# Kernel optimization log

Hardware: AMD Instinct MI355X
Metric: run time of the kernel (lower is better)

The kernel has to match this reference:

```python
import jax, jax.numpy as jnp
import numpy as np

UNITS = 256   # wiring.units (state size)
OUT = 64      # wiring.output_dim (motor neurons = last OUT units)


def setup_inputs() -> dict:
    key = jax.random.key(0)
    k_x, k_wi, k_wr, k_mi, k_mr = jax.random.split(key, 5)
    B, L, C = 32, 8192, 128
    x = jax.random.normal(k_x, (B, L, C), dtype=jnp.float32)
    # learned parameters
    W_in = jax.random.normal(k_wi, (C, UNITS), dtype=jnp.float32) * 0.05
    W_rec = jax.random.normal(k_wr, (UNITS, UNITS), dtype=jnp.float32) * 0.05
    b = jnp.zeros((UNITS,), dtype=jnp.float32)
    # fixed sparse wiring masks (sensory adjacency [C,U], recurrent adjacency [U,U])
    M_in = jax.random.bernoulli(k_mi, 0.5, (C, UNITS)).astype(jnp.float32)
    M_rec = jax.random.bernoulli(k_mr, 0.5, (UNITS, UNITS)).astype(jnp.float32)
    return {"x": x, "W_in": W_in, "W_rec": W_rec, "b": b, "M_in": M_in, "M_rec": M_rec}


def reference(x, W_in, W_rec, b, M_in, M_rec):
    # Pre-apply the wiring sparsity masks once (original masks weights each step).
    Wi = W_in * M_in          # [C, U]
    Wr = W_rec * M_rec        # [U, U]
    B = x.shape[0]
    h0 = jnp.zeros((B, UNITS), dtype=x.dtype)
    xT = jnp.swapaxes(x, 0, 1)  # [L, B, C] -> scan over time

    def step(h, xt):
        h_new = jnp.tanh(xt @ Wi + h @ Wr + b)   # wired RNN cell, tanh nonlinearity
        # output_size < state_size: emit only motor neurons (last OUT units)
        return h_new, h_new[:, UNITS - OUT:]

    h_last, ys = jax.lax.scan(step, h0, xT)      # ys: [L, B, OUT]
    readout = jnp.swapaxes(ys, 0, 1)             # [B, L, OUT] (batch_first, return_sequences)
    return readout, h_last
```

## Files before the change

kernel.cpp:

```cpp
#include <hip/hip_runtime.h>
#include <hip/hip_bf16.h>
#include <stdint.h>


#define NB 32
#define SL 8192
#define NC 128
#define NU 256
#define NO 64
#define NK 384
#define GR 64

typedef _Float16 h16;
typedef __attribute__((ext_vector_type(2))) _Float16 h16x2;

__device__ __forceinline__ float fdot2f(h16x2 a, h16x2 b, float c) {
#if __has_builtin(__builtin_amdgcn_fdot2)
    return __builtin_amdgcn_fdot2(a, b, c, false);
#else
    return c + (float)a[0] * (float)b[0] + (float)a[1] * (float)b[1];
#endif
}

__device__ __forceinline__ float ftanh(float x) {
#if __has_builtin(__builtin_amdgcn_exp2f) && __has_builtin(__builtin_amdgcn_rcpf)
    float e = __builtin_amdgcn_exp2f(x * 2.8853900817779268f);
    return 1.0f - 2.0f * __builtin_amdgcn_rcpf(e + 1.0f);
#else
    return tanhf(x);
#endif
}

__global__ __launch_bounds__(256, 4) void xw_gemm_kernel(
    const float* __restrict__ x,
    const float* __restrict__ W_in,
    const float* __restrict__ bias,
    const float* __restrict__ M_in,
    h16* __restrict__ xw)
{
    const int u = threadIdx.x;
    const long row0 = (long)blockIdx.x * GR;
    __shared__ h16 xs[GR * NC];

    for (int i = u; i < GR * NC; i += 256)
        xs[i] = (h16)x[row0 * NC + i];

    h16x2 wc[NC / 2];
#pragma unroll
    for (int j = 0; j < NC / 2; ++j) {
        const int k0 = 2 * j, k1 = 2 * j + 1;
        float w0 = W_in[k0 * NU + u] * M_in[k0 * NU + u];
        float w1 = W_in[k1 * NU + u] * M_in[k1 * NU + u];
        h16x2 t; t[0] = (h16)w0; t[1] = (h16)w1;
        wc[j] = t;
    }
    const float bs = bias[u];
    __syncthreads();

    for (int r = 0; r < GR; ++r) {
        const h16x2* xv = (const h16x2*)&xs[r * NC];
        float acc = bs;
#pragma unroll
        for (int j = 0; j < NC / 2; ++j)
            acc = fdot2f(xv[j], wc[j], acc);
        xw[(row0 + r) * NU + u] = (h16)acc;
    }
}

__global__ __launch_bounds__(512, 2) void rnn_scan_xw(
    const float* __restrict__ W_rec,
    const float* __restrict__ M_rec,
    const h16* __restrict__ xw,
    float* __restrict__ out)
{
    const int tid  = threadIdx.x;
    const int b    = blockIdx.x;
    const int lane = tid & 63;
    const int wv   = tid >> 6;
    const int u    = (wv << 5) | (lane & 31);
    const int kc   = lane >> 5;
    const int ks   = kc << 7;

    __shared__ __align__(16) h16 vec[2][NU];

    h16x2 w[64];
#pragma unroll
    for (int j = 0; j < 64; ++j) {
        const int k0 = ks + 2 * j, k1 = k0 + 1;
        float w0 = W_rec[k0 * NU + u] * M_rec[k0 * NU + u];
        float w1 = W_rec[k1 * NU + u] * M_rec[k1 * NU + u];
        h16x2 t; t[0] = (h16)w0; t[1] = (h16)w1;
        w[j] = t;
    }

    if (tid < NU) vec[0][tid] = (h16)0.f;
    __syncthreads();

    const h16* __restrict__ xwb = xw + (long)b * SL * NU;
    long off = u;
    float xwv = (float)xwb[off];

    float* const outb = out + (long)b * SL * NO;
    const int uo = u - (NU - NO);

    for (int t = 0; t < SL; ++t) {
        const long offn = (t + 1 < SL) ? off + (long)NU : off;
        const float xwn = (float)xwb[offn];

        const h16x2* v2 = (const h16x2*)(&vec[t & 1][ks]);
        float a0 = 0.f, a1 = 0.f, a2 = 0.f, a3 = 0.f;
#pragma unroll
        for (int j = 0; j < 16; ++j) {
            a0 = fdot2f(v2[4 * j + 0], w[4 * j + 0], a0);
            a1 = fdot2f(v2[4 * j + 1], w[4 * j + 1], a1);
            a2 = fdot2f(v2[4 * j + 2], w[4 * j + 2], a2);
            a3 = fdot2f(v2[4 * j + 3], w[4 * j + 3], a3);
        }
        float s = (a0 + a1) + (a2 + a3);
        if (kc) s += xwv;
        s += __shfl_xor(s, 32, 64);

        const float hn = ftanh(s);
        if (kc == 0) {
            vec[(t + 1) & 1][u] = (h16)hn;
            if (t == SL - 1)
                out[(long)NB * SL * NO + (long)b * NU + u] = hn;
        } else if (uo >= 0) {
            outb[(long)t * NO + uo] = hn;
        }
        __syncthreads();
        off = offn; xwv = xwn;
    }
}

__global__ __launch_bounds__(1024, 4) void rnn_scan_fallback(
    const float* __restrict__ x,
    const float* __restrict__ W_in,
    const float* __restrict__ W_rec,
    const float* __restrict__ bias,
    const float* __restrict__ M_in,
    const float* __restrict__ M_rec,
    float* __restrict__ out)
{
    const int tid = threadIdx.x;
    const int b   = blockIdx.x;
    const int u   = tid & (NU - 1);
    const int kc  = tid >> 8;
    const int ks  = kc * 96;

    __shared__ __align__(16) h16 vec[NK];
    __shared__ float partial[4][NU];

    h16x2 w[48];
#pragma unroll
    for (int j = 0; j < 48; ++j) {
        const int k0 = ks + 2 * j, k1 = k0 + 1;
        float w0, w1;
        if (k0 < NU) w0 = W_rec[k0 * NU + u] * M_rec[k0 * NU + u];
        else         w0 = W_in[(k0 - NU) * NU + u] * M_in[(k0 - NU) * NU + u];
        if (k1 < NU) w1 = W_rec[k1 * NU + u] * M_rec[k1 * NU + u];
        else         w1 = W_in[(k1 - NU) * NU + u] * M_in[(k1 - NU) * NU + u];
        h16x2 t; t[0] = (h16)w0; t[1] = (h16)w1;
        w[j] = t;
    }
    const float breg = (tid < NU) ? bias[u] : 0.0f;
    const long xbase = (long)b * SL * NC;

    if (tid < NU) vec[tid] = (h16)0.f;
    else if (tid < NU + NC) vec[tid] = (h16)x[xbase + (tid - NU)];
    __syncthreads();

    const bool xthr = (tid >= NU) && (tid < NU + NC);
    for (int t = 0; t < SL; ++t) {
        float xr = 0.f;
        if (xthr && (t + 1 < SL)) xr = x[xbase + (long)(t + 1) * NC + (tid - NU)];

        const h16x2* v2 = (const h16x2*)(&vec[ks]);
        float acc = 0.f;
#pragma unroll
        for (int j = 0; j < 48; ++j) acc = fdot2f(v2[j], w[j], acc);
        partial[kc][u] = acc;
        __syncthreads();

        if (tid < NU) {
            float s = partial[0][u] + partial[1][u] + partial[2][u] + partial[3][u] + breg;
            float hn = ftanh(s);
            vec[u] = (h16)hn;
            if (u >= NU - NO) out[((long)b * SL + t) * NO + (u - (NU - NO))] = hn;
            if (t == SL - 1)  out[(long)NB * SL * NO + (long)b * NU + u] = hn;
        } else if (xthr && (t + 1 < SL)) {
            vec[tid] = (h16)xr;
        }
        __syncthreads();
    }
}

extern "C" void kernel_launch(void* const* d_in, const int* in_sizes, int n_in,
                              void* d_out, int out_size, void* d_ws, size_t ws_size,
                              hipStream_t stream) {
    (void)in_sizes; (void)n_in; (void)out_size;
    const float* x     = (const float*)d_in[0];
    const float* W_in  = (const float*)d_in[1];
    const float* W_rec = (const float*)d_in[2];
    const float* bias  = (const float*)d_in[3];
    const float* M_in  = (const float*)d_in[4];
    const float* M_rec = (const float*)d_in[5];
    float* out = (float*)d_out;

    const size_t xw_bytes = (size_t)NB * SL * NU * sizeof(h16);
    if (ws_size >= xw_bytes) {
        h16* xw = (h16*)d_ws;
        xw_gemm_kernel<<<dim3((NB * SL) / GR), dim3(256), 0, stream>>>(x, W_in, bias, M_in, xw);
        rnn_scan_xw<<<dim3(NB), dim3(512), 0, stream>>>(W_rec, M_rec, xw, out);
    } else {
        rnn_scan_fallback<<<dim3(NB), dim3(1024), 0, stream>>>(x, W_in, W_rec, bias, M_in, M_rec, out);
    }
}
```

Baseline: 4.595 ms.

## Stage xw in shared-memory chunks and batch output stores in the scan

The scan kernel now copies the precomputed input projection into a double-buffered shared-memory chunk of 16 timesteps with one 16-byte load per thread, prefetched a chunk ahead. This replaces a per-step scalar global load of xw. Output stores are buffered in registers and written once per chunk, which moves global memory traffic off the serial per-step critical path. The GEMM inner loop also uses four accumulators to break the dependency chain. The costs are higher register pressure from sbuf and some extra shared memory.

```diff
diff --git a/kernel.cpp b/kernel.cpp
--- a/kernel.cpp
+++ b/kernel.cpp
@@ -10,6 +10,8 @@
 #define NO 64
 #define NK 384
 #define GR 64
+#define TC 16
+#define NCHUNK (SL / TC)
 
 typedef _Float16 h16;
 typedef __attribute__((ext_vector_type(2))) _Float16 h16x2;
@@ -59,11 +61,15 @@
 
     for (int r = 0; r < GR; ++r) {
         const h16x2* xv = (const h16x2*)&xs[r * NC];
-        float acc = bs;
-#pragma unroll
-        for (int j = 0; j < NC / 2; ++j)
-            acc = fdot2f(xv[j], wc[j], acc);
-        xw[(row0 + r) * NU + u] = (h16)acc;
+        float a0 = bs, a1 = 0.f, a2 = 0.f, a3 = 0.f;
+#pragma unroll
+        for (int j = 0; j < 16; ++j) {
+            a0 = fdot2f(xv[4 * j + 0], wc[4 * j + 0], a0);
+            a1 = fdot2f(xv[4 * j + 1], wc[4 * j + 1], a1);
+            a2 = fdot2f(xv[4 * j + 2], wc[4 * j + 2], a2);
+            a3 = fdot2f(xv[4 * j + 3], wc[4 * j + 3], a3);
+        }
+        xw[(row0 + r) * NU + u] = (h16)((a0 + a1) + (a2 + a3));
     }
 }
 
@@ -82,6 +88,7 @@
     const int ks   = kc << 7;
 
     __shared__ __align__(16) h16 vec[2][NU];
+    __shared__ __align__(16) h16 xwc[2][TC][NU];
 
     h16x2 w[64];
 #pragma unroll
@@ -93,43 +100,56 @@
         w[j] = t;
     }
 
-    if (tid < NU) vec[0][tid] = (h16)0.f;
-    __syncthreads();
-
     const h16* __restrict__ xwb = xw + (long)b * SL * NU;
-    long off = u;
-    float xwv = (float)xwb[off];
-
     float* const outb = out + (long)b * SL * NO;
     const int uo = u - (NU - NO);
 
-    for (int t = 0; t < SL; ++t) {
-        const long offn = (t + 1 < SL) ? off + (long)NU : off;
-        const float xwn = (float)xwb[offn];
-
-        const h16x2* v2 = (const h16x2*)(&vec[t & 1][ks]);
-        float a0 = 0.f, a1 = 0.f, a2 = 0.f, a3 = 0.f;
-#pragma unroll
-        for (int j = 0; j < 16; ++j) {
-            a0 = fdot2f(v2[4 * j + 0], w[4 * j + 0], a0);
-            a1 = fdot2f(v2[4 * j + 1], w[4 * j + 1], a1);
-            a2 = fdot2f(v2[4 * j + 2], w[4 * j + 2], a2);
-            a3 = fdot2f(v2[4 * j + 3], w[4 * j + 3], a3);
+    {
+        const int4 c0 = ((const int4*)xwb)[tid];
+        if (tid < NU) vec[0][tid] = (h16)0.f;
+        ((int4*)&xwc[0][0][0])[tid] = c0;
+        __syncthreads();
+    }
+
+    for (int tc = 0; tc < NCHUNK; ++tc) {
+        const int cb = tc & 1;
+        const bool havenext = (tc + 1 < NCHUNK);
+        int4 creg;
+        if (havenext)
+            creg = ((const int4*)(xwb + (long)(tc + 1) * TC * NU))[tid];
+        float sbuf[TC];
+
+#pragma unroll
+        for (int j = 0; j < TC; ++j) {
+            const h16x2* v2 = (const h16x2*)(&vec[j & 1][ks]);
+            float a0 = 0.f, a1 = 0.f, a2 = 0.f, a3 = 0.f;
+#pragma unroll
+            for (int q = 0; q < 16; ++q) {
+                a0 = fdot2f(v2[4 * q + 0], w[4 * q + 0], a0);
+                a1 = fdot2f(v2[4 * q + 1], w[4 * q + 1], a1);
+                a2 = fdot2f(v2[4 * q + 2], w[4 * q + 2], a2);
+                a3 = fdot2f(v2[4 * q + 3], w[4 * q + 3], a3);
+            }
+            float s = (a0 + a1) + (a2 + a3);
+            if (kc) s += (float)xwc[cb][j][u];
+            s += __shfl_xor(s, 32, 64);
+
+            const float hn = ftanh(s);
+            if (kc == 0) vec[(j + 1) & 1][u] = (h16)hn;
+            sbuf[j] = hn;
+
+            if (j == TC - 1) {
+                if (havenext) ((int4*)&xwc[cb ^ 1][0][0])[tid] = creg;
+                if (kc == 1 && uo >= 0) {
+#pragma unroll
+                    for (int jj = 0; jj < TC; ++jj)
+                        outb[(long)(tc * TC + jj) * NO + uo] = sbuf[jj];
+                }
+                if (tc == NCHUNK - 1 && kc == 0)
+                    out[(long)NB * SL * NO + (long)b * NU + u] = hn;
+            }
+            __syncthreads();
         }
-        float s = (a0 + a1) + (a2 + a3);
-        if (kc) s += xwv;
-        s += __shfl_xor(s, 32, 64);
-
-        const float hn = ftanh(s);
-        if (kc == 0) {
-            vec[(t + 1) & 1][u] = (h16)hn;
-            if (t == SL - 1)
-                out[(long)NB * SL * NO + (long)b * NU + u] = hn;
-        } else if (uo >= 0) {
-            outb[(long)t * NO + uo] = hn;
-        }
-        __syncthreads();
-        off = offn; xwv = xwn;
     }
 }
 
```

Result: no change. 4.532 ms (-1.4%).
